# Kernel tuning notes

Hardware: AMD Instinct MI355X
Metric: run time of the kernel (lower is better)

Reference implementation:

```python
import jax, jax.numpy as jnp
import numpy as np

WIDTH = 8  # fixed-point fractional bits (init arg Width)


def quantizer(x, width=WIDTH):
    # Fixed-point quantization to `width` fractional bits, clipped to [-1, 1].
    scale = jnp.asarray(2.0 ** width, x.dtype)
    return jnp.clip(jnp.round(x * scale) / scale, -1.0, 1.0)


def setup_inputs() -> dict:
    key = jax.random.key(0)
    k1, k2, k3 = jax.random.split(key, 3)
    N, H, W, C = 32, 56, 56, 128
    KH, KW, F = 3, 3, 256
    OH, OW = H - KH + 1, W - KW + 1  # valid padding, stride 1
    x = jax.random.normal(k1, (N, H, W, C), dtype=jnp.float32) * 0.5
    kernels = jax.random.normal(k2, (KH, KW, C, F), dtype=jnp.float32) * 0.01
    bias = jax.random.normal(k3, (OH, OW, F), dtype=jnp.float32) * 0.01
    return {"x": x, "kernels": kernels, "bias": bias}


def reference(x, kernels, bias):
    # Method == 'Fixed': quantize input and kernels, valid conv, quantize output,
    # then per-position bias add + ReLU.
    xq = quantizer(x)
    wq = quantizer(kernels)
    out = jax.lax.conv_general_dilated(
        xq, wq,
        window_strides=(1, 1),
        padding="VALID",
        dimension_numbers=("NHWC", "HWIO", "NHWC"),
    )
    out = quantizer(out)
    return jax.nn.relu(out + bias[None, :, :, :])
```

## Files before the change

### kernel.cpp

```cpp
#include <hip/hip_runtime.h>
#include <hip/hip_bf16.h>
#include <stdint.h>
#include <stddef.h>


typedef float  f32x4  __attribute__((ext_vector_type(4)));
typedef short  bf16x8 __attribute__((ext_vector_type(8)));

#define N_IMG 32
#define H_IN 56
#define W_IN 56
#define C_IN 128
#define F_OUT 256
#define OHW 54
#define M_TOTAL (N_IMG * OHW * OHW)
#define BM 128
#define BN 128
#define BK 64

__device__ __forceinline__ unsigned short quant_to_bf16(float x) {
    float a = rintf(x * 256.0f);
    a = fminf(fmaxf(a, -256.0f), 256.0f);
    float q = a * 0.00390625f;
    union { float f; unsigned int u; } cv; cv.f = q;
    return (unsigned short)(cv.u >> 16);
}

__device__ __forceinline__ void async_copy16(const unsigned short* g, unsigned short* l) {
    __builtin_amdgcn_global_load_lds(
        (const __attribute__((address_space(1))) unsigned int*)g,
        (__attribute__((address_space(3))) unsigned int*)l, 16, 0, 0);
}

__global__ __launch_bounds__(256) void quant_x_kernel(
        const float* __restrict__ x, unsigned short* __restrict__ xq) {
    int i = (blockIdx.x * 256 + threadIdx.x) * 4;
    float4 v = *reinterpret_cast<const float4*>(x + i);
    ushort4 o;
    o.x = quant_to_bf16(v.x);
    o.y = quant_to_bf16(v.y);
    o.z = quant_to_bf16(v.z);
    o.w = quant_to_bf16(v.w);
    *reinterpret_cast<ushort4*>(xq + i) = o;
}

__global__ __launch_bounds__(256) void quant_w_kernel(
        const float* __restrict__ w, unsigned short* __restrict__ wp) {
    int idx = blockIdx.x * 256 + threadIdx.x;
    int c  = idx & 127;
    int f  = (idx >> 7) & 255;
    int kk = idx >> 15;
    wp[idx] = quant_to_bf16(w[(kk * C_IN + c) * F_OUT + f]);
}

__global__ __launch_bounds__(256, 2) void conv_kernel(
        const unsigned short* __restrict__ xq,
        const unsigned short* __restrict__ wp,
        const float* __restrict__ bias,
        float* __restrict__ out)
{
    __shared__ __attribute__((aligned(16))) unsigned short Alds[2][BM * BK];
    __shared__ __attribute__((aligned(16))) unsigned short Blds[2][BN * BK];

    const int tid  = threadIdx.x;
    const int wave = tid >> 6;
    const int lane = tid & 63;
    const int bid  = blockIdx.x;
    const int mb   = bid >> 1;
    const int nb   = bid & 1;
    const int m0   = mb * BM;
    const int wr   = wave >> 1;
    const int wc   = wave & 1;

    const int row0 = tid >> 3;
    const int sw   = (tid & 7) ^ (row0 & 7);
    const int dstc = (tid & ~63) * 8;

    const unsigned short* a_base[4];
#pragma unroll
    for (int r = 0; r < 4; ++r) {
        int m = m0 + row0 + 32 * r;
        int n_img = m / (OHW * OHW);
        int rem   = m % (OHW * OHW);
        int oh = rem / OHW, ow = rem % OHW;
        a_base[r] = xq + (size_t)((n_img * H_IN + oh) * W_IN + ow) * C_IN + sw * 8;
    }
    const unsigned short* b_base[4];
#pragma unroll
    for (int r = 0; r < 4; ++r)
        b_base[r] = wp + (size_t)(nb * BN + row0 + 32 * r) * C_IN + sw * 8;

    auto stage = [&](int t, unsigned short* Ab, unsigned short* Bb) {
        int kk = t >> 1, hf = t & 1;
        int kh = (kk * 43) >> 7, kw = kk - 3 * kh;
        int aoff = (kh * W_IN + kw) * C_IN + hf * 64;
        int boff = kk * (F_OUT * C_IN) + hf * 64;
#pragma unroll
        for (int r = 0; r < 4; ++r)
            async_copy16(a_base[r] + aoff, Ab + r * 2048 + dstc);
#pragma unroll
        for (int r = 0; r < 4; ++r)
            async_copy16(b_base[r] + boff, Bb + r * 2048 + dstc);
    };

    const int mr = lane & 15;
    const int lq = lane >> 4;

    f32x4 acc[4][4];
#pragma unroll
    for (int i = 0; i < 4; ++i)
#pragma unroll
        for (int j = 0; j < 4; ++j) acc[i][j] = (f32x4)(0.0f);

    auto compute = [&](const unsigned short* Ab, const unsigned short* Bb) {
#pragma unroll
        for (int ks = 0; ks < 2; ++ks) {
            const int ch = (((ks * 4 + lq) ^ (mr & 7)) * 8);
            bf16x8 af[4], bfr[4];
#pragma unroll
            for (int mi = 0; mi < 4; ++mi)
                af[mi] = *reinterpret_cast<const bf16x8*>(
                    Ab + (wr * 64 + mi * 16 + mr) * BK + ch);
#pragma unroll
            for (int ni = 0; ni < 4; ++ni)
                bfr[ni] = *reinterpret_cast<const bf16x8*>(
                    Bb + (wc * 64 + ni * 16 + mr) * BK + ch);
#pragma unroll
            for (int mi = 0; mi < 4; ++mi)
#pragma unroll
                for (int ni = 0; ni < 4; ++ni)
                    acc[mi][ni] = __builtin_amdgcn_mfma_f32_16x16x32_bf16(
                        af[mi], bfr[ni], acc[mi][ni], 0, 0, 0);
        }
    };

    stage(0, Alds[0], Blds[0]);
    __syncthreads();

#pragma unroll 1
    for (int tp = 0; tp < 8; ++tp) {
        stage(2 * tp + 1, Alds[1], Blds[1]);
        compute(Alds[0], Blds[0]);
        __syncthreads();
        stage(2 * tp + 2, Alds[0], Blds[0]);
        compute(Alds[1], Blds[1]);
        __syncthreads();
    }
    stage(17, Alds[1], Blds[1]);
    compute(Alds[0], Blds[0]);
    __syncthreads();
    compute(Alds[1], Blds[1]);

    const int fcol0 = nb * BN + wc * 64 + mr;
#pragma unroll
    for (int mi = 0; mi < 4; ++mi) {
#pragma unroll
        for (int rr = 0; rr < 4; ++rr) {
            const int m = m0 + wr * 64 + mi * 16 + lq * 4 + rr;
            const float* brow = bias + (size_t)(m % (OHW * OHW)) * F_OUT;
            float* orow = out + (size_t)m * F_OUT;
#pragma unroll
            for (int ni = 0; ni < 4; ++ni) {
                float v = acc[mi][ni][rr];
                float t = rintf(v * 256.0f);
                t = fminf(fmaxf(t, -256.0f), 256.0f);
                float o = t * 0.00390625f + brow[fcol0 + ni * 16];
                orow[fcol0 + ni * 16] = fmaxf(o, 0.0f);
            }
        }
    }
}

extern "C" void kernel_launch(void* const* d_in, const int* in_sizes, int n_in,
                              void* d_out, int out_size, void* d_ws, size_t ws_size,
                              hipStream_t stream) {
    (void)in_sizes; (void)n_in; (void)out_size;
    const float* x    = (const float*)d_in[0];
    const float* w    = (const float*)d_in[1];
    const float* bias = (const float*)d_in[2];
    float* out        = (float*)d_out;

    const size_t x_elems = (size_t)N_IMG * H_IN * W_IN * C_IN;
    const size_t w_elems = (size_t)9 * F_OUT * C_IN;
    const size_t xq_bytes = x_elems * sizeof(unsigned short);
    const size_t need = xq_bytes + w_elems * sizeof(unsigned short);
    if (ws_size < need) return;

    unsigned short* xq = (unsigned short*)d_ws;
    unsigned short* wp = (unsigned short*)((char*)d_ws + xq_bytes);

    quant_x_kernel<<<(int)(x_elems / (256 * 4)), 256, 0, stream>>>(x, xq);
    quant_w_kernel<<<(int)(w_elems / 256), 256, 0, stream>>>(w, wp);
    conv_kernel<<<(M_TOTAL / BM) * 2, 256, 0, stream>>>(xq, wp, bias, out);
}
```

Before: 96.00 us.

## Prepack weights in MFMA fragment order and load B directly into registers

The weight quantization kernel now writes weights pre-permuted into the per-lane MFMA B-fragment layout. The conv kernel drops the B tile from LDS and loads each wave's B fragments straight from global memory (L2-resident) into double-buffered registers, one step ahead of compute. This halves LDS usage and LDS traffic per step. In exchange it raises register pressure and redundantly reads B per wave (wr duplicates), with global load latency exposed instead of hidden by async LDS copies.

```diff
diff --git a/kernel.cpp b/kernel.cpp
--- a/kernel.cpp
+++ b/kernel.cpp
@@ -45,22 +45,26 @@
 }
 
 __global__ __launch_bounds__(256) void quant_w_kernel(
-        const float* __restrict__ w, unsigned short* __restrict__ wp) {
+        const float* __restrict__ w, unsigned short* __restrict__ wpf) {
     int idx = blockIdx.x * 256 + threadIdx.x;
-    int c  = idx & 127;
-    int f  = (idx >> 7) & 255;
+    int j  = idx & 7;
+    int l  = (idx >> 3) & 63;
+    int g  = (idx >> 9) & 15;
+    int ks = (idx >> 13) & 1;
+    int hf = (idx >> 14) & 1;
     int kk = idx >> 15;
-    wp[idx] = quant_to_bf16(w[(kk * C_IN + c) * F_OUT + f]);
+    int f  = g * 16 + (l & 15);
+    int c  = hf * 64 + ks * 32 + (l >> 4) * 8 + j;
+    wpf[idx] = quant_to_bf16(w[(kk * C_IN + c) * F_OUT + f]);
 }
 
 __global__ __launch_bounds__(256, 2) void conv_kernel(
         const unsigned short* __restrict__ xq,
-        const unsigned short* __restrict__ wp,
+        const unsigned short* __restrict__ wpf,
         const float* __restrict__ bias,
         float* __restrict__ out)
 {
     __shared__ __attribute__((aligned(16))) unsigned short Alds[2][BM * BK];
-    __shared__ __attribute__((aligned(16))) unsigned short Blds[2][BN * BK];
 
     const int tid  = threadIdx.x;
     const int wave = tid >> 6;
@@ -85,22 +89,34 @@
         int oh = rem / OHW, ow = rem % OHW;
         a_base[r] = xq + (size_t)((n_img * H_IN + oh) * W_IN + ow) * C_IN + sw * 8;
     }
-    const unsigned short* b_base[4];
-#pragma unroll
-    for (int r = 0; r < 4; ++r)
-        b_base[r] = wp + (size_t)(nb * BN + row0 + 32 * r) * C_IN + sw * 8;
-
-    auto stage = [&](int t, unsigned short* Ab, unsigned short* Bb) {
+
+    auto stageA = [&](int t, unsigned short* Ab) {
         int kk = t >> 1, hf = t & 1;
         int kh = (kk * 43) >> 7, kw = kk - 3 * kh;
         int aoff = (kh * W_IN + kw) * C_IN + hf * 64;
-        int boff = kk * (F_OUT * C_IN) + hf * 64;
 #pragma unroll
         for (int r = 0; r < 4; ++r)
             async_copy16(a_base[r] + aoff, Ab + r * 2048 + dstc);
-#pragma unroll
-        for (int r = 0; r < 4; ++r)
-            async_copy16(b_base[r] + boff, Bb + r * 2048 + dstc);
+    };
+
+    const unsigned short* b_base = wpf + (size_t)(nb * 8 + wc * 4) * 512 + lane * 8;
+
+    bf16x8 bregA[4][2], bregB[4][2];
+    auto loadB_A = [&](int t) {
+#pragma unroll
+        for (int ni = 0; ni < 4; ++ni)
+#pragma unroll
+            for (int ks = 0; ks < 2; ++ks)
+                bregA[ni][ks] = *reinterpret_cast<const bf16x8*>(
+                    b_base + t * 16384 + ks * 8192 + ni * 512);
+    };
+    auto loadB_B = [&](int t) {
+#pragma unroll
+        for (int ni = 0; ni < 4; ++ni)
+#pragma unroll
+            for (int ks = 0; ks < 2; ++ks)
+                bregB[ni][ks] = *reinterpret_cast<const bf16x8*>(
+                    b_base + t * 16384 + ks * 8192 + ni * 512);
     };
 
     const int mr = lane & 15;
@@ -112,44 +128,61 @@
 #pragma unroll
         for (int j = 0; j < 4; ++j) acc[i][j] = (f32x4)(0.0f);
 
-    auto compute = [&](const unsigned short* Ab, const unsigned short* Bb) {
+    auto computeA = [&](const unsigned short* Ab) {
 #pragma unroll
         for (int ks = 0; ks < 2; ++ks) {
             const int ch = (((ks * 4 + lq) ^ (mr & 7)) * 8);
-            bf16x8 af[4], bfr[4];
+            bf16x8 af[4];
 #pragma unroll
             for (int mi = 0; mi < 4; ++mi)
                 af[mi] = *reinterpret_cast<const bf16x8*>(
                     Ab + (wr * 64 + mi * 16 + mr) * BK + ch);
 #pragma unroll
-            for (int ni = 0; ni < 4; ++ni)
-                bfr[ni] = *reinterpret_cast<const bf16x8*>(
-                    Bb + (wc * 64 + ni * 16 + mr) * BK + ch);
-#pragma unroll
             for (int mi = 0; mi < 4; ++mi)
 #pragma unroll
                 for (int ni = 0; ni < 4; ++ni)
                     acc[mi][ni] = __builtin_amdgcn_mfma_f32_16x16x32_bf16(
-                        af[mi], bfr[ni], acc[mi][ni], 0, 0, 0);
+                        af[mi], bregA[ni][ks], acc[mi][ni], 0, 0, 0);
         }
     };
-
-    stage(0, Alds[0], Blds[0]);
+    auto computeB = [&](const unsigned short* Ab) {
+#pragma unroll
+        for (int ks = 0; ks < 2; ++ks) {
+            const int ch = (((ks * 4 + lq) ^ (mr & 7)) * 8);
+            bf16x8 af[4];
+#pragma unroll
+            for (int mi = 0; mi < 4; ++mi)
+                af[mi] = *reinterpret_cast<const bf16x8*>(
+                    Ab + (wr * 64 + mi * 16 + mr) * BK + ch);
+#pragma unroll
+            for (int mi = 0; mi < 4; ++mi)
+#pragma unroll
+                for (int ni = 0; ni < 4; ++ni)
+                    acc[mi][ni] = __builtin_amdgcn_mfma_f32_16x16x32_bf16(
+                        af[mi], bregB[ni][ks], acc[mi][ni], 0, 0, 0);
+        }
+    };
+
+    stageA(0, Alds[0]);
+    loadB_A(0);
     __syncthreads();
 
 #pragma unroll 1
     for (int tp = 0; tp < 8; ++tp) {
-        stage(2 * tp + 1, Alds[1], Blds[1]);
-        compute(Alds[0], Blds[0]);
+        stageA(2 * tp + 1, Alds[1]);
+        loadB_B(2 * tp + 1);
+        computeA(Alds[0]);
         __syncthreads();
-        stage(2 * tp + 2, Alds[0], Blds[0]);
-        compute(Alds[1], Blds[1]);
+        stageA(2 * tp + 2, Alds[0]);
+        loadB_A(2 * tp + 2);
+        computeB(Alds[1]);
         __syncthreads();
     }
-    stage(17, Alds[1], Blds[1]);
-    compute(Alds[0], Blds[0]);
+    stageA(17, Alds[1]);
+    loadB_B(17);
+    computeA(Alds[0]);
     __syncthreads();
-    compute(Alds[1], Blds[1]);
+    computeB(Alds[1]);
 
     const int fcol0 = nb * BN + wc * 64 + mr;
 #pragma unroll
@@ -186,10 +219,10 @@
     const size_t need = xq_bytes + w_elems * sizeof(unsigned short);
     if (ws_size < need) return;
 
-    unsigned short* xq = (unsigned short*)d_ws;
-    unsigned short* wp = (unsigned short*)((char*)d_ws + xq_bytes);
+    unsigned short* xq  = (unsigned short*)d_ws;
+    unsigned short* wpf = (unsigned short*)((char*)d_ws + xq_bytes);
 
     quant_x_kernel<<<(int)(x_elems / (256 * 4)), 256, 0, stream>>>(x, xq);
-    quant_w_kernel<<<(int)(w_elems / 256), 256, 0, stream>>>(w, wp);
-    conv_kernel<<<(M_TOTAL / BM) * 2, 256, 0, stream>>>(xq, wp, bias, out);
-}
+    quant_w_kernel<<<(int)(w_elems / 256), 256, 0, stream>>>(w, wpf);
+    conv_kernel<<<(M_TOTAL / BM) * 2, 256, 0, stream>>>(xq, wpf, bias, out);
+}
```

New measurement: 86.85 us. -9.5%, faster.
